# Optimization experiments

Hardware: AMD Instinct MI355X
Metric: run time of the kernel (lower is better)

Reference implementation:

```python
import jax, jax.numpy as jnp
import numpy as np

B, S, D, E = 4, 2048, 2048, 8


def setup_inputs() -> dict:
    key = jax.random.key(0)
    ks = jax.random.split(key, 5)
    scale = 1.0 / np.sqrt(D)
    x = jax.random.normal(ks[0], (B, S, D), dtype=jnp.float32)
    # experts: torch Linear stores W as [out, in]; y = x @ W.T + b
    expert_w = jax.random.uniform(ks[1], (E, D, D), dtype=jnp.float32, minval=-scale, maxval=scale)
    expert_b = jax.random.uniform(ks[2], (E, D), dtype=jnp.float32, minval=-scale, maxval=scale)
    router_w = jax.random.uniform(ks[3], (E, D), dtype=jnp.float32, minval=-scale, maxval=scale)
    router_b = jax.random.uniform(ks[4], (E,), dtype=jnp.float32, minval=-scale, maxval=scale)
    return {"x": x, "expert_w": expert_w, "expert_b": expert_b,
            "router_w": router_w, "router_b": router_b}


def reference(x, expert_w, expert_b, router_w, router_b):
    b, s, d = x.shape
    n_exp = expert_w.shape[0]
    xf = x.reshape(b * s, d)                       # [N, D]
    logits = xf @ router_w.T + router_b            # [N, E]
    probs = jax.nn.softmax(logits, axis=-1)
    expert_id = jnp.argmax(probs, axis=-1)         # [N] top-1 routing
    top_prob = jnp.max(probs, axis=-1)             # [N] gate weight
    out = jnp.zeros_like(xf)
    # dense-equivalent of the masked gather/scatter: each expert's linear
    # applied to all tokens, masked by routing decision (E is small & static)
    for i in range(n_exp):
        y = xf @ expert_w[i].T + expert_b[i]       # [N, D]
        out = out + jnp.where((expert_id == i)[:, None], y, 0.0)
    out = out * top_prob[:, None]
    # forward never calls compute_loss; returns loss = 0
    return out.reshape(b, s, d), jnp.float32(0.0)
```

## Files before the change

kernel.cpp:

```cpp
#include <hip/hip_runtime.h>
#include <hip/hip_bf16.h>

#define N_TOK 8192
#define DIM   2048
#define NEXP  8
#define BM    288
#define BN    256
#define BK    32
#define NT    (DIM / BK)
#define NBLK  256

#define A_BYTES  (BM * BK * 2)
#define B_BYTES  (BN * BK * 4)
#define RING     (A_BYTES + B_BYTES)
#define DYN_LDS  (3 * RING)

typedef __attribute__((ext_vector_type(8))) short  short8;
typedef __attribute__((ext_vector_type(4))) float  f32x4;
typedef __attribute__((ext_vector_type(4))) unsigned int u32x4;

static __device__ __forceinline__ unsigned int pack_bf2(float a, float b) {
  union { __hip_bfloat16 h; unsigned short u; } ca, cb;
  ca.h = __float2bfloat16(a);
  cb.h = __float2bfloat16(b);
  return ((unsigned int)cb.u << 16) | (unsigned int)ca.u;
}

static __device__ __forceinline__ void gload16(const void* g, void* l) {
  __builtin_amdgcn_global_load_lds(
      (const __attribute__((address_space(1))) unsigned int*)g,
      (__attribute__((address_space(3))) unsigned int*)l, 16, 0, 0);
}

static __device__ __forceinline__ double dot8d(const float4& x0, const float4& x1,
                                               const float4& w0, const float4& w1) {
  double a = 0.0;
  a = fma((double)x0.x, (double)w0.x, a);
  a = fma((double)x0.y, (double)w0.y, a);
  a = fma((double)x0.z, (double)w0.z, a);
  a = fma((double)x0.w, (double)w0.w, a);
  a = fma((double)x1.x, (double)w1.x, a);
  a = fma((double)x1.y, (double)w1.y, a);
  a = fma((double)x1.z, (double)w1.z, a);
  a = fma((double)x1.w, (double)w1.w, a);
  return a;
}

__global__ __launch_bounds__(256, 3) void router_kernel(
    const float* __restrict__ x, const float* __restrict__ rw,
    const float* __restrict__ rb, int* __restrict__ eid,
    float* __restrict__ gate, unsigned short* __restrict__ xb)
{
  const int t    = threadIdx.x;
  const int tok0 = blockIdx.x * 4;

  float4 w0[NEXP], w1[NEXP];
#pragma unroll
  for (int e = 0; e < NEXP; e++) {
    const float4* wr = reinterpret_cast<const float4*>(rw + (size_t)e * DIM);
    w0[e] = wr[2 * t];
    w1[e] = wr[2 * t + 1];
  }
  float4 xv0[4], xv1[4];
#pragma unroll
  for (int k = 0; k < 4; k++) {
    const float4* xr = reinterpret_cast<const float4*>(x + (size_t)(tok0 + k) * DIM);
    xv0[k] = xr[2 * t];
    xv1[k] = xr[2 * t + 1];
  }
#pragma unroll
  for (int k = 0; k < 4; k++) {
    u32x4 pk;
    pk[0] = pack_bf2(xv0[k].x, xv0[k].y); pk[1] = pack_bf2(xv0[k].z, xv0[k].w);
    pk[2] = pack_bf2(xv1[k].x, xv1[k].y); pk[3] = pack_bf2(xv1[k].z, xv1[k].w);
    *reinterpret_cast<u32x4*>(xb + (size_t)(tok0 + k) * DIM + t * 8) = pk;
  }

  __shared__ double red[4][4][NEXP];
  const int lane = t & 63, wv = t >> 6;
#pragma unroll
  for (int k = 0; k < 4; k++) {
    double s[NEXP];
#pragma unroll
    for (int e = 0; e < NEXP; e++) s[e] = dot8d(xv0[k], xv1[k], w0[e], w1[e]);
#pragma unroll
    for (int e = 0; e < NEXP; e++) {
      double v = s[e];
#pragma unroll
      for (int off = 32; off > 0; off >>= 1) v += __shfl_xor(v, off, 64);
      if (lane == 0) red[wv][k][e] = v;
    }
  }
  __syncthreads();
  if (t < 4) {
    double lg[NEXP];
    double lmax = -1e300; int best = 0;
#pragma unroll
    for (int e = 0; e < NEXP; e++) {
      lg[e] = red[0][t][e] + red[1][t][e] + red[2][t][e] + red[3][t][e] + (double)rb[e];
      if (lg[e] > lmax) { lmax = lg[e]; best = e; }
    }
    float den = 0.f;
#pragma unroll
    for (int e = 0; e < NEXP; e++) den += expf((float)(lg[e] - lmax));
    eid[tok0 + t]  = best;
    gate[tok0 + t] = 1.0f / den;
  }
}

__global__ __launch_bounds__(1024) void histo_perm(
    const int* __restrict__ eid, int* __restrict__ counts, int* __restrict__ perm)
{
  __shared__ int hist[NEXP], baseS[NEXP], fillS[NEXP];
  const int t = threadIdx.x;
  if (t < NEXP) { hist[t] = 0; fillS[t] = 0; }
  __syncthreads();
  int my[8];
#pragma unroll
  for (int i = 0; i < 8; i++) {
    my[i] = eid[t + i * 1024];
    atomicAdd(&hist[my[i]], 1);
  }
  __syncthreads();
  if (t == 0) {
    int b = 0;
#pragma unroll
    for (int e = 0; e < NEXP; e++) { counts[e] = hist[e]; baseS[e] = b; b += hist[e]; }
  }
  __syncthreads();
#pragma unroll
  for (int i = 0; i < 8; i++) {
    int pos = baseS[my[i]] + atomicAdd(&fillS[my[i]], 1);
    perm[pos] = t + i * 1024;
  }
}

__global__ __launch_bounds__(512, 2) void moe_gemm(
    const unsigned short* __restrict__ xb, const float* __restrict__ ew,
    const float* __restrict__ eb, const float* __restrict__ gate,
    const int* __restrict__ perm, const int* __restrict__ counts,
    float* __restrict__ out)
{
  extern __shared__ char smem[];
  __shared__ int   aRowS[BM];
  __shared__ float gateS[BM];

  const int tid  = threadIdx.x;
  const int lane = tid & 63, wid = tid >> 6;

  int ttot = 0;
#pragma unroll
  for (int j = 0; j < NEXP; j++) ttot += (counts[j] + BM - 1) / BM;
  ttot *= 8;
  const int tq = ttot >> 3, tr = ttot & 7;

  const int nA5 = (wid < 2);
  int aR0[3];
  aR0[0] = (wid * 2) * 16;
  aR0[1] = (wid * 2 + 1) * 16;
  aR0[2] = nA5 ? ((16 + wid) * 16) : aR0[0];
  int aDst[3];
#pragma unroll
  for (int i = 0; i < 3; i++) aDst[i] = aR0[i] * 64;
  const int lrowA = lane >> 2;
  const int cblkA = (lane & 3) ^ ((lane >> 3) & 3);

  int bR0[4];
#pragma unroll
  for (int i = 0; i < 4; i++) bR0[i] = wid * 32 + i * 8;
  int bDst[4];
#pragma unroll
  for (int i = 0; i < 4; i++) bDst[i] = A_BYTES + bR0[i] * 128;
  const int lrowB = lane >> 3;
  const int cblkB = (lane & 7) ^ (lrowB & 7);

  const int l15 = lane & 15;
  const int wr = wid >> 2, wc = wid & 3;
  const int swA  = (((lane >> 4) ^ ((l15 >> 1) & 3)) * 16);
  const int aOff = (wr * 144 + l15) * 64 + swA;
  const int csB  = (lane >> 4) * 2;
  int bOffN[4];
#pragma unroll
  for (int n = 0; n < 4; n++) {
    int row = wc * 64 + n * 16 + l15;
    bOffN[n] = A_BYTES + row * 128 + ((csB ^ (row & 7)) << 4);
  }
  const int rsub = (lane >> 4) * 4;

  for (int ti = blockIdx.x; ti < ttot; ti += NBLK) {
    const int k  = ti & 7, j = ti >> 3;
    const int tt = k * tq + (k < tr ? k : tr) + j;
    const int bx = tt >> 3, by = tt & 7;

    int e = 0, rowbase = 0, nrows = 0, found = 0;
    {
      int tsum = 0, bsum = 0;
#pragma unroll
      for (int jj = 0; jj < NEXP; jj++) {
        int cj = counts[jj];
        int te = (cj + BM - 1) / BM;
        if (!found && bx < tsum + te) {
          int loc = bx - tsum;
          e = jj;
          rowbase = bsum + loc * BM;
          int rem = cj - loc * BM;
          nrows = rem < BM ? rem : BM;
          found = 1;
        }
        tsum += te; bsum += cj;
      }
    }

    __syncthreads();
    if (tid < BM) {
      int idx = tid < nrows ? tid : (nrows - 1);
      int tok = perm[rowbase + idx];
      aRowS[tid] = tok;
      gateS[tid] = gate[tok];
    }
    __syncthreads();

    const float* wB32 = ew + (size_t)e * DIM * DIM;
    const unsigned short* aSrc[3];
    const float* bSrc[4];
#pragma unroll
    for (int i = 0; i < 3; i++)
      aSrc[i] = xb + (size_t)aRowS[aR0[i] + lrowA] * DIM + cblkA * 8;
#pragma unroll
    for (int i = 0; i < 4; i++)
      bSrc[i] = wB32 + (size_t)(by * BN + bR0[i] + lrowB) * DIM + cblkB * 4;

#define STAGE(SLOTP)                                                        \
    do {                                                                    \
      char* sb_ = (SLOTP);                                                  \
      gload16(aSrc[0], sb_ + aDst[0]);                                      \
      gload16(aSrc[1], sb_ + aDst[1]);                                      \
      if (nA5) gload16(aSrc[2], sb_ + aDst[2]);                             \
      gload16(bSrc[0], sb_ + bDst[0]);                                      \
      gload16(bSrc[1], sb_ + bDst[1]);                                      \
      gload16(bSrc[2], sb_ + bDst[2]);                                      \
      gload16(bSrc[3], sb_ + bDst[3]);                                      \
      aSrc[0] += BK; aSrc[1] += BK; aSrc[2] += BK;                          \
      bSrc[0] += BK; bSrc[1] += BK; bSrc[2] += BK; bSrc[3] += BK;           \
    } while (0)

    STAGE(smem);
    STAGE(smem + RING);

    f32x4 acc[9][4] = {};

#pragma unroll 1
    for (int t = 0; t < NT; ++t) {
      if (t < NT - 1) {
        if (nA5) asm volatile("s_waitcnt vmcnt(7)" ::: "memory");
        else     asm volatile("s_waitcnt vmcnt(6)" ::: "memory");
      } else {
        asm volatile("s_waitcnt vmcnt(0)" ::: "memory");
      }
      __builtin_amdgcn_s_barrier();

      if (t + 2 < NT) {
        int slot = t + 2;
        slot -= (slot >= 3) ? 3 : 0;
        slot -= (slot >= 3) ? 3 : 0;
        STAGE(smem + (size_t)((t + 2) % 3) * RING);
        (void)slot;
      }

      const char* cur = smem + (size_t)(t % 3) * RING;

      f32x4 r0[4], r1[4];
#pragma unroll
      for (int n = 0; n < 4; n++) {
        r0[n] = *(const f32x4*)(cur + bOffN[n]);
        r1[n] = *(const f32x4*)(cur + (bOffN[n] ^ 16));
      }
      short8 bf[4];
#pragma unroll
      for (int n = 0; n < 4; n++) {
        u32x4 pk;
        pk[0] = pack_bf2(r0[n][0], r0[n][1]);
        pk[1] = pack_bf2(r0[n][2], r0[n][3]);
        pk[2] = pack_bf2(r1[n][0], r1[n][1]);
        pk[3] = pack_bf2(r1[n][2], r1[n][3]);
        union { u32x4 u; short8 s; } cv;
        cv.u = pk;
        bf[n] = cv.s;
      }
      short8 af[9];
#pragma unroll
      for (int m = 0; m < 9; m++) af[m] = *(const short8*)(cur + aOff + m * 1024);

      __builtin_amdgcn_s_setprio(1);
#pragma unroll
      for (int m = 0; m < 9; m++)
#pragma unroll
        for (int n = 0; n < 4; n++)
          acc[m][n] = __builtin_amdgcn_mfma_f32_16x16x32_bf16(af[m], bf[n], acc[m][n], 0, 0, 0);
      __builtin_amdgcn_s_setprio(0);
    }
#undef STAGE

    const int cb = by * BN + wc * 64;
    const float* ebE = eb + (size_t)e * DIM;
    float bias[4];
#pragma unroll
    for (int n = 0; n < 4; n++) bias[n] = ebE[cb + n * 16 + l15];
#pragma unroll
    for (int m = 0; m < 9; m++) {
      int r0w = wr * 144 + m * 16 + rsub;
#pragma unroll
      for (int rg = 0; rg < 4; rg++) {
        int r = r0w + rg;
        if (r < nrows) {
          float g = gateS[r];
          float* orow = out + (size_t)aRowS[r] * DIM + cb;
#pragma unroll
          for (int n = 0; n < 4; n++)
            orow[n * 16 + l15] = (acc[m][n][rg] + bias[n]) * g;
        }
      }
    }
    asm volatile("s_waitcnt vmcnt(0)" ::: "memory");
  }
}

extern "C" void kernel_launch(void* const* d_in, const int* in_sizes, int n_in,
                              void* d_out, int out_size, void* d_ws, size_t ws_size,
                              hipStream_t stream)
{
  const float* x  = (const float*)d_in[0];
  const float* ew = (const float*)d_in[1];
  const float* eb = (const float*)d_in[2];
  const float* rw = (const float*)d_in[3];
  const float* rb = (const float*)d_in[4];
  float* out = (float*)d_out;

  char* ws = (char*)d_ws;
  int*   eid    = (int*)(ws);
  float* gate   = (float*)(ws + 32 * 1024);
  int*   counts = (int*)(ws + 64 * 1024);
  int*   perm   = (int*)(ws + 128 * 1024);
  unsigned short* xbuf = (unsigned short*)(ws + 192 * 1024);

  hipFuncSetAttribute(reinterpret_cast<const void*>(moe_gemm),
                      hipFuncAttributeMaxDynamicSharedMemorySize, DYN_LDS);

  hipMemsetAsync(out + (size_t)N_TOK * DIM, 0, sizeof(float), stream);
  router_kernel<<<N_TOK / 4, 256, 0, stream>>>(x, rw, rb, eid, gate, xbuf);
  histo_perm<<<1, 1024, 0, stream>>>(eid, counts, perm);
  moe_gemm<<<NBLK, 512, DYN_LDS, stream>>>(xbuf, ew, eb, gate, perm, counts, out);
}
```

Measured before the change: 155.3 us.

## Halve GEMM N-tile to 128 with 256-thread blocks and double buffering

The expert GEMM moves from BN=256 with 512 threads and a 3-stage LDS ring to BN=128 with 256 threads and a 2-stage ring, doubling the tile count and launching 512 blocks. The load mapping and the wave layout change to match. The goal is more resident blocks and better load balance across CUs, at the cost of more A-tile reloads (each A tile is now reused over half as many columns) and less prefetch depth, since every iteration waits on vmcnt(0). The separate memset of the loss slot is folded into the histogram kernel to save one launch.

Result: no change. 153.7 us (-1.0%).

```diff
diff --git a/kernel.cpp b/kernel.cpp
--- a/kernel.cpp
+++ b/kernel.cpp
@@ -5,15 +5,15 @@
 #define DIM   2048
 #define NEXP  8
 #define BM    288
-#define BN    256
+#define BN    128
 #define BK    32
 #define NT    (DIM / BK)
-#define NBLK  256
+#define NBLK  512
 
 #define A_BYTES  (BM * BK * 2)
 #define B_BYTES  (BN * BK * 4)
 #define RING     (A_BYTES + B_BYTES)
-#define DYN_LDS  (3 * RING)
+#define DYN_LDS  (2 * RING)
 
 typedef __attribute__((ext_vector_type(8))) short  short8;
 typedef __attribute__((ext_vector_type(4))) float  f32x4;
@@ -109,11 +109,13 @@
 }
 
 __global__ __launch_bounds__(1024) void histo_perm(
-    const int* __restrict__ eid, int* __restrict__ counts, int* __restrict__ perm)
+    const int* __restrict__ eid, int* __restrict__ counts, int* __restrict__ perm,
+    float* __restrict__ out)
 {
   __shared__ int hist[NEXP], baseS[NEXP], fillS[NEXP];
   const int t = threadIdx.x;
   if (t < NEXP) { hist[t] = 0; fillS[t] = 0; }
+  if (t == 64) out[(size_t)N_TOK * DIM] = 0.0f;
   __syncthreads();
   int my[8];
 #pragma unroll
@@ -135,7 +137,7 @@
   }
 }
 
-__global__ __launch_bounds__(512, 2) void moe_gemm(
+__global__ __launch_bounds__(256, 2) void moe_gemm(
     const unsigned short* __restrict__ xb, const float* __restrict__ ew,
     const float* __restrict__ eb, const float* __restrict__ gate,
     const int* __restrict__ perm, const int* __restrict__ counts,
@@ -151,31 +153,31 @@
   int ttot = 0;
 #pragma unroll
   for (int j = 0; j < NEXP; j++) ttot += (counts[j] + BM - 1) / BM;
-  ttot *= 8;
+  ttot *= 16;
   const int tq = ttot >> 3, tr = ttot & 7;
 
   const int nA5 = (wid < 2);
-  int aR0[3];
-  aR0[0] = (wid * 2) * 16;
-  aR0[1] = (wid * 2 + 1) * 16;
-  aR0[2] = nA5 ? ((16 + wid) * 16) : aR0[0];
-  int aDst[3];
-#pragma unroll
-  for (int i = 0; i < 3; i++) aDst[i] = aR0[i] * 64;
+  int aC[5];
+#pragma unroll
+  for (int i = 0; i < 5; i++)
+    aC[i] = (wid < 2) ? (wid * 5 + i) : (10 + (wid - 2) * 4 + ((i < 4) ? i : 0));
+  int aDst[5];
+#pragma unroll
+  for (int i = 0; i < 5; i++) aDst[i] = aC[i] * 1024;
   const int lrowA = lane >> 2;
   const int cblkA = (lane & 3) ^ ((lane >> 3) & 3);
 
-  int bR0[4];
-#pragma unroll
-  for (int i = 0; i < 4; i++) bR0[i] = wid * 32 + i * 8;
+  int bC[4];
+#pragma unroll
+  for (int i = 0; i < 4; i++) bC[i] = wid * 4 + i;
   int bDst[4];
 #pragma unroll
-  for (int i = 0; i < 4; i++) bDst[i] = A_BYTES + bR0[i] * 128;
+  for (int i = 0; i < 4; i++) bDst[i] = A_BYTES + bC[i] * 1024;
   const int lrowB = lane >> 3;
   const int cblkB = (lane & 7) ^ (lrowB & 7);
 
   const int l15 = lane & 15;
-  const int wr = wid >> 2, wc = wid & 3;
+  const int wr = wid >> 1, wc = wid & 1;
   const int swA  = (((lane >> 4) ^ ((l15 >> 1) & 3)) * 16);
   const int aOff = (wr * 144 + l15) * 64 + swA;
   const int csB  = (lane >> 4) * 2;
@@ -190,7 +192,7 @@
   for (int ti = blockIdx.x; ti < ttot; ti += NBLK) {
     const int k  = ti & 7, j = ti >> 3;
     const int tt = k * tq + (k < tr ? k : tr) + j;
-    const int bx = tt >> 3, by = tt & 7;
+    const int bx = tt >> 4, by = tt & 15;
 
     int e = 0, rowbase = 0, nrows = 0, found = 0;
     {
@@ -212,62 +214,53 @@
     }
 
     __syncthreads();
-    if (tid < BM) {
-      int idx = tid < nrows ? tid : (nrows - 1);
+    for (int r = tid; r < BM; r += 256) {
+      int idx = r < nrows ? r : (nrows - 1);
       int tok = perm[rowbase + idx];
-      aRowS[tid] = tok;
-      gateS[tid] = gate[tok];
+      aRowS[r] = tok;
+      gateS[r] = gate[tok];
     }
     __syncthreads();
 
     const float* wB32 = ew + (size_t)e * DIM * DIM;
-    const unsigned short* aSrc[3];
+    const unsigned short* aSrc[5];
     const float* bSrc[4];
 #pragma unroll
-    for (int i = 0; i < 3; i++)
-      aSrc[i] = xb + (size_t)aRowS[aR0[i] + lrowA] * DIM + cblkA * 8;
+    for (int i = 0; i < 5; i++)
+      aSrc[i] = xb + (size_t)aRowS[aC[i] * 16 + lrowA] * DIM + cblkA * 8;
 #pragma unroll
     for (int i = 0; i < 4; i++)
-      bSrc[i] = wB32 + (size_t)(by * BN + bR0[i] + lrowB) * DIM + cblkB * 4;
+      bSrc[i] = wB32 + (size_t)(by * BN + bC[i] * 8 + lrowB) * DIM + cblkB * 4;
 
 #define STAGE(SLOTP)                                                        \
     do {                                                                    \
       char* sb_ = (SLOTP);                                                  \
       gload16(aSrc[0], sb_ + aDst[0]);                                      \
       gload16(aSrc[1], sb_ + aDst[1]);                                      \
-      if (nA5) gload16(aSrc[2], sb_ + aDst[2]);                             \
+      gload16(aSrc[2], sb_ + aDst[2]);                                      \
+      gload16(aSrc[3], sb_ + aDst[3]);                                      \
+      if (nA5) gload16(aSrc[4], sb_ + aDst[4]);                             \
       gload16(bSrc[0], sb_ + bDst[0]);                                      \
       gload16(bSrc[1], sb_ + bDst[1]);                                      \
       gload16(bSrc[2], sb_ + bDst[2]);                                      \
       gload16(bSrc[3], sb_ + bDst[3]);                                      \
-      aSrc[0] += BK; aSrc[1] += BK; aSrc[2] += BK;                          \
+      aSrc[0] += BK; aSrc[1] += BK; aSrc[2] += BK; aSrc[3] += BK;           \
+      aSrc[4] += BK;                                                        \
       bSrc[0] += BK; bSrc[1] += BK; bSrc[2] += BK; bSrc[3] += BK;           \
     } while (0)
 
     STAGE(smem);
-    STAGE(smem + RING);
 
     f32x4 acc[9][4] = {};
 
 #pragma unroll 1
     for (int t = 0; t < NT; ++t) {
-      if (t < NT - 1) {
-        if (nA5) asm volatile("s_waitcnt vmcnt(7)" ::: "memory");
-        else     asm volatile("s_waitcnt vmcnt(6)" ::: "memory");
-      } else {
-        asm volatile("s_waitcnt vmcnt(0)" ::: "memory");
-      }
+      asm volatile("s_waitcnt vmcnt(0)" ::: "memory");
       __builtin_amdgcn_s_barrier();
 
-      if (t + 2 < NT) {
-        int slot = t + 2;
-        slot -= (slot >= 3) ? 3 : 0;
-        slot -= (slot >= 3) ? 3 : 0;
-        STAGE(smem + (size_t)((t + 2) % 3) * RING);
-        (void)slot;
-      }
-
-      const char* cur = smem + (size_t)(t % 3) * RING;
+      if (t + 1 < NT) STAGE(smem + (size_t)((t + 1) & 1) * RING);
+
+      const char* cur = smem + (size_t)(t & 1) * RING;
 
       f32x4 r0[4], r1[4];
 #pragma unroll
@@ -346,8 +339,7 @@
   hipFuncSetAttribute(reinterpret_cast<const void*>(moe_gemm),
                       hipFuncAttributeMaxDynamicSharedMemorySize, DYN_LDS);
 
-  hipMemsetAsync(out + (size_t)N_TOK * DIM, 0, sizeof(float), stream);
   router_kernel<<<N_TOK / 4, 256, 0, stream>>>(x, rw, rb, eid, gate, xbuf);
-  histo_perm<<<1, 1024, 0, stream>>>(eid, counts, perm);
-  moe_gemm<<<NBLK, 512, DYN_LDS, stream>>>(xbuf, ew, eb, gate, perm, counts, out);
-}
+  histo_perm<<<1, 1024, 0, stream>>>(eid, counts, perm, out);
+  moe_gemm<<<NBLK, 256, DYN_LDS, stream>>>(xbuf, ew, eb, gate, perm, counts, out);
+}
```
